# Optimization experiments

Hardware: AMD Instinct MI355X
Metric: run time of the kernel (lower is better)

Reference implementation:

```python
import jax, jax.numpy as jnp
import numpy as np

B, S, E, H = 2, 2048, 1024, 16
D = E // H  # head_dim = 64


def _rope(x):
    # x: (B, H, S, D); torchtune-style interleaved rotary embedding
    s, d = x.shape[-2], x.shape[-1]
    inv_freq = 1.0 / (10000.0 ** (jnp.arange(0, d, 2, dtype=jnp.float32) / d))  # (d/2,)
    freqs = jnp.arange(s, dtype=jnp.float32)[:, None] * inv_freq[None, :]       # (S, d/2)
    cos, sin = jnp.cos(freqs), jnp.sin(freqs)
    x1, x2 = x[..., 0::2], x[..., 1::2]
    o1 = x1 * cos - x2 * sin
    o2 = x2 * cos + x1 * sin
    return jnp.stack([o1, o2], axis=-1).reshape(x.shape)


def setup_inputs() -> dict:
    key = jax.random.key(0)
    kx, kq, kk, kv, ko = jax.random.split(key, 5)
    std = 1.0 / np.sqrt(E)
    return {
        "x": jax.random.normal(kx, (B, S, E), dtype=jnp.float32),
        "W_q": jax.random.normal(kq, (E, E), dtype=jnp.float32) * std,
        "W_k": jax.random.normal(kk, (E, E), dtype=jnp.float32) * std,
        "W_v": jax.random.normal(kv, (E, E), dtype=jnp.float32) * std,
        "W_o": jax.random.normal(ko, (E, E), dtype=jnp.float32) * std,
    }


def reference(x, W_q, W_k, W_v, W_o):
    b, s, e = x.shape
    h, d = H, e // H
    # nn.Linear: y = x @ W.T  (weights are (out, in))
    q = (x @ W_q.T).reshape(b, s, h, d).transpose(0, 2, 1, 3)  # (B,H,S,D)
    k = (x @ W_k.T).reshape(b, s, h, d).transpose(0, 2, 1, 3)
    v = (x @ W_v.T).reshape(b, s, h, d).transpose(0, 2, 1, 3)
    q = _rope(q)
    k = _rope(k)
    attn_scale = 1.0 / np.sqrt(e)  # NOTE: scales by sqrt(hidden_dim), as in source
    scores = jnp.einsum("bhsd,bhtd->bhst", q, k) * attn_scale  # (B,H,S,S)
    causal = jnp.triu(jnp.ones((s, s), dtype=bool), k=1)
    scores = jnp.where(causal, -jnp.inf, scores)
    probs = jax.nn.softmax(scores, axis=-1)  # dropout is identity in eval
    out = jnp.einsum("bhst,bhtd->bhsd", probs, v)
    out = out.transpose(0, 2, 1, 3).reshape(b, s, e)
    return out @ W_o.T
```

## Files before the change

### kernel.cpp

```cpp
#include <hip/hip_runtime.h>
#include <hip/hip_bf16.h>

#define BATCH 2
#define SEQ   2048
#define EMB   1024
#define NH    16
#define HD    64
#define MROWS (BATCH*SEQ)
#define NX    (MROWS*EMB)
#define NW    (EMB*EMB)

using f32x4  = __attribute__((ext_vector_type(4))) float;
using bf16x8 = __attribute__((ext_vector_type(8))) short;

#define GLOBAL_AS(p) ((const __attribute__((address_space(1))) void*)(p))
#define LDS_AS(p)    ((__attribute__((address_space(3))) void*)(p))

#define ROPE_L2 0.4152410118609203f
#define QSCALE  0.045084220027780106f

__global__ void fused_cast_kernel(const float* __restrict__ x,
                                  const float* __restrict__ Wq,
                                  const float* __restrict__ Wk,
                                  const float* __restrict__ Wv,
                                  const float* __restrict__ Wo,
                                  __hip_bfloat16* __restrict__ xb,
                                  __hip_bfloat16* __restrict__ Wqkvb,
                                  __hip_bfloat16* __restrict__ Wob,
                                  float2* __restrict__ ctab) {
    if (blockIdx.x >= 4096) {
        int e  = (blockIdx.x - 4096) * 256 + threadIdx.x;
        int s  = e >> 5;
        int ip = e & 31;
        float inv = exp2f(-(float)ip * ROPE_L2);
        float fr  = (float)s * inv;
        float2 cs;
        cs.x = cosf(fr);
        cs.y = sinf(fr);
        ctab[e] = cs;
        return;
    }
    size_t i8 = (size_t)(blockIdx.x * 256 + threadIdx.x) * 8;
    const float* src;
    __hip_bfloat16* dst;
    if (i8 < (size_t)NX) {
        src = x + i8;
        dst = xb + i8;
    } else {
        size_t w = i8 - NX;
        int which = (int)(w >> 20);
        size_t local = w & (NW - 1);
        if (which < 3) {
            src = (which == 0 ? Wq : (which == 1 ? Wk : Wv)) + local;
            dst = Wqkvb + w;
        } else {
            src = Wo + local;
            dst = Wob + local;
        }
    }
    float4 a = *(const float4*)(src);
    float4 b = *(const float4*)(src + 4);
    union { uint4 u; ushort s[8]; } o;
    const float* f = (const float*)&a;
#pragma unroll
    for (int j = 0; j < 4; ++j) {
        __hip_bfloat16 h = __float2bfloat16(f[j]);
        o.s[j] = *(ushort*)&h;
    }
    f = (const float*)&b;
#pragma unroll
    for (int j = 0; j < 4; ++j) {
        __hip_bfloat16 h = __float2bfloat16(f[j]);
        o.s[4 + j] = *(ushort*)&h;
    }
    *(uint4*)dst = o.u;
}

__global__ __launch_bounds__(256) void gemm_qkv_kernel(
        const __hip_bfloat16* __restrict__ A,
        const __hip_bfloat16* __restrict__ W,
        __hip_bfloat16* __restrict__ Qo,
        __hip_bfloat16* __restrict__ Ko,
        __hip_bfloat16* __restrict__ Vo,
        const float2* __restrict__ ctab, int M, int K) {
    __shared__ __hip_bfloat16 As[128 * 64];
    __shared__ __hip_bfloat16 Bs[128 * 64];

    const int tid  = threadIdx.x;
    const int wave = tid >> 6;
    const int lane = tid & 63;
    const int quad = lane >> 4;
    const int l16  = lane & 15;
    const int m0   = blockIdx.y * 128;
    const int n0   = blockIdx.x * 128;
    const int wm   = (wave >> 1) * 64;
    const int wn   = (wave & 1) * 64;
    const int xr   = l16 & 7;

    f32x4 acc[4][4] = {};

    for (int k0 = 0; k0 < K; k0 += 64) {
#pragma unroll
        for (int it = 0; it < 4; ++it) {
            int flat = (wave * 4 + it) * 64 + lane;
            int row  = flat >> 3;
            int g    = (flat & 7) ^ (row & 7);
            const __hip_bfloat16* ga = A + (size_t)(m0 + row) * K + k0 + g * 8;
            const __hip_bfloat16* gb = W + (size_t)(n0 + row) * K + k0 + g * 8;
            __builtin_amdgcn_global_load_lds(GLOBAL_AS(ga),
                LDS_AS(As + (size_t)(wave * 4 + it) * 512), 16, 0, 0);
            __builtin_amdgcn_global_load_lds(GLOBAL_AS(gb),
                LDS_AS(Bs + (size_t)(wave * 4 + it) * 512), 16, 0, 0);
        }
        __syncthreads();

#pragma unroll
        for (int kk = 0; kk < 2; ++kk) {
            const int kg = (kk * 4 + quad) ^ xr;
            bf16x8 af[4], bfr[4];
#pragma unroll
            for (int i = 0; i < 4; ++i) {
                af[i]  = *(const bf16x8*)(&As[(wm + i * 16 + l16) * 64 + kg * 8]);
                bfr[i] = *(const bf16x8*)(&Bs[(wn + i * 16 + l16) * 64 + kg * 8]);
            }
#pragma unroll
            for (int i = 0; i < 4; ++i)
#pragma unroll
                for (int j = 0; j < 4; ++j)
                    acc[i][j] = __builtin_amdgcn_mfma_f32_16x16x32_bf16(
                        af[i], bfr[j], acc[i][j], 0, 0, 0);
        }
        __syncthreads();
    }

    const int tens = n0 >> 10;
    __hip_bfloat16* outp = (tens == 0) ? Qo : ((tens == 1) ? Ko : Vo);
    const int nbase = n0 & 1023;
    if (tens < 2) {
        const float sgn   = (l16 & 1) ? 1.0f : -1.0f;
        const float qmul  = (tens == 0) ? QSCALE : 1.0f;
#pragma unroll
        for (int i = 0; i < 4; ++i)
#pragma unroll
            for (int j = 0; j < 4; ++j) {
                int col  = nbase + wn + j * 16 + l16;
                int ip   = ((wn + j * 16 + l16) & 63) >> 1;
                int row0 = m0 + wm + i * 16 + quad * 4;
#pragma unroll
                for (int rr = 0; rr < 4; ++rr) {
                    float v = acc[i][j][rr];
                    float p = __shfl_xor(v, 1);
                    int sp  = (row0 + rr) & (SEQ - 1);
                    float2 cs = ctab[sp * 32 + ip];
                    float o = (v * cs.x + sgn * p * cs.y) * qmul;
                    outp[(size_t)(row0 + rr) * EMB + col] = __float2bfloat16(o);
                }
            }
    } else {
#pragma unroll
        for (int i = 0; i < 4; ++i)
#pragma unroll
            for (int j = 0; j < 4; ++j) {
                int col  = nbase + wn + j * 16 + l16;
                int row0 = m0 + wm + i * 16 + quad * 4;
#pragma unroll
                for (int rr = 0; rr < 4; ++rr)
                    outp[(size_t)(row0 + rr) * EMB + col] = __float2bfloat16(acc[i][j][rr]);
            }
    }
}

__global__ __launch_bounds__(256) void gemm_oproj_kernel(
        const __hip_bfloat16* __restrict__ A,
        const __hip_bfloat16* __restrict__ Bm,
        float* __restrict__ C, int M, int N, int K) {
    __shared__ __hip_bfloat16 As[128 * 64];
    __shared__ __hip_bfloat16 Bs[64 * 64];

    const int tid  = threadIdx.x;
    const int wave = tid >> 6;
    const int lane = tid & 63;
    const int quad = lane >> 4;
    const int l16  = lane & 15;
    const int m0   = blockIdx.y * 128;
    const int n0   = blockIdx.x * 64;
    const int wm   = (wave >> 1) * 64;
    const int wn   = (wave & 1) * 32;
    const int xr   = l16 & 7;

    f32x4 acc[4][2] = {};

    for (int k0 = 0; k0 < K; k0 += 64) {
#pragma unroll
        for (int it = 0; it < 4; ++it) {
            int flat = (wave * 4 + it) * 64 + lane;
            int row  = flat >> 3;
            int g    = (flat & 7) ^ (row & 7);
            const __hip_bfloat16* ga = A + (size_t)(m0 + row) * K + k0 + g * 8;
            __builtin_amdgcn_global_load_lds(GLOBAL_AS(ga),
                LDS_AS(As + (size_t)(wave * 4 + it) * 512), 16, 0, 0);
        }
#pragma unroll
        for (int it = 0; it < 2; ++it) {
            int flat = (wave * 2 + it) * 64 + lane;
            int row  = flat >> 3;
            int g    = (flat & 7) ^ (row & 7);
            const __hip_bfloat16* gb = Bm + (size_t)(n0 + row) * K + k0 + g * 8;
            __builtin_amdgcn_global_load_lds(GLOBAL_AS(gb),
                LDS_AS(Bs + (size_t)(wave * 2 + it) * 512), 16, 0, 0);
        }
        __syncthreads();

#pragma unroll
        for (int kk = 0; kk < 2; ++kk) {
            const int kg = (kk * 4 + quad) ^ xr;
            bf16x8 af[4], bfr[2];
#pragma unroll
            for (int i = 0; i < 4; ++i)
                af[i] = *(const bf16x8*)(&As[(wm + i * 16 + l16) * 64 + kg * 8]);
#pragma unroll
            for (int j = 0; j < 2; ++j)
                bfr[j] = *(const bf16x8*)(&Bs[(wn + j * 16 + l16) * 64 + kg * 8]);
#pragma unroll
            for (int i = 0; i < 4; ++i)
#pragma unroll
                for (int j = 0; j < 2; ++j)
                    acc[i][j] = __builtin_amdgcn_mfma_f32_16x16x32_bf16(
                        af[i], bfr[j], acc[i][j], 0, 0, 0);
        }
        __syncthreads();
    }

#pragma unroll
    for (int i = 0; i < 4; ++i)
#pragma unroll
        for (int j = 0; j < 2; ++j) {
            int col  = n0 + wn + j * 16 + l16;
            int row0 = m0 + wm + i * 16 + quad * 4;
#pragma unroll
            for (int rr = 0; rr < 4; ++rr)
                C[(size_t)(row0 + rr) * N + col] = acc[i][j][rr];
        }
}

__device__ inline uint cvt_pk_bf16(float lo, float hi) {
    uint r;
    asm("v_cvt_pk_bf16_f32 %0, %1, %2" : "=v"(r) : "v"(lo), "v"(hi));
    return r;
}
__device__ inline float exp2_raw(float x) {
    float r;
    asm("v_exp_f32 %0, %1" : "=v"(r) : "v"(x));
    return r;
}

__global__ __launch_bounds__(512) void attn_mfma_kernel(
        const __hip_bfloat16* __restrict__ Qb,
        const __hip_bfloat16* __restrict__ Kb,
        const __hip_bfloat16* __restrict__ Vb,
        __hip_bfloat16* __restrict__ Attnb) {
    const int di   = blockIdx.y * 16 + blockIdx.x;
    const int qt   = 15 - (di >> 5);
    const int bh   = di & 31;
    const int b    = bh >> 4;
    const int h    = bh & (NH - 1);
    const int tid  = threadIdx.x;
    const int wave = tid >> 6;
    const int lane = tid & 63;
    const int quad = lane >> 4;
    const int l16  = lane & 15;

    __shared__ __hip_bfloat16 Ks[2][64 * 64];
    __shared__ uint VTs[2][64][33];

    const int pc   = tid >> 4;
    const int sgg  = tid & 15;
    const int d0   = sgg * 4;
    const int lr   = lane >> 3;
    const int lg   = (lane & 7) ^ lr;
    const size_t ksrc_lane = (size_t)lr * EMB + lg * 8;

    const __hip_bfloat16* Kbase = Kb + (size_t)b * SEQ * EMB + h * HD;
    const __hip_bfloat16* Vbase = Vb + (size_t)b * SEQ * EMB + h * HD;

    union { uint u[4]; bf16x8 v; } onesu;
    onesu.u[0] = 0x3F803F80u; onesu.u[1] = 0x3F803F80u;
    onesu.u[2] = 0x3F803F80u; onesu.u[3] = 0x3F803F80u;
    const bf16x8 ones = onesu.v;

    const int  nt      = 2 * qt + 2;
    const bool lowHalf = (wave < 4);
    const int  we      = lowHalf ? wave : wave - 4;

    const int qrow0 = qt * 128 + wave * 16;
    bf16x8 qf[2];
    {
        const __hip_bfloat16* qp =
            Qb + (size_t)(b * SEQ + qrow0 + l16) * EMB + h * HD + quad * 8;
        qf[0] = *(const bf16x8*)(qp);
        qf[1] = *(const bf16x8*)(qp + 32);
    }

    f32x4 of[4]  = {};
    f32x4 of_sum = {};

    const __hip_bfloat16* kgp = Kbase;
    const __hip_bfloat16* vgp = Vbase + (size_t)(2 * pc) * EMB + d0;
    uint2 va = *(const uint2*)(vgp);
    uint2 vb = *(const uint2*)(vgp + EMB);
    __builtin_amdgcn_global_load_lds(
        GLOBAL_AS(kgp + (size_t)(8 * wave) * EMB + ksrc_lane),
        LDS_AS(&Ks[0][wave * 512]), 16, 0, 0);

    for (int i = 0; i < nt; ++i) {
        const int cur = i & 1;

        {
            const uint* vau = (const uint*)&va;
            const uint* vbu = (const uint*)&vb;
#pragma unroll
            for (int j = 0; j < 2; ++j) {
                VTs[cur][d0 + 2 * j][pc] =
                    __builtin_amdgcn_perm(vbu[j], vau[j], 0x05040100u);
                VTs[cur][d0 + 2 * j + 1][pc] =
                    __builtin_amdgcn_perm(vbu[j], vau[j], 0x07060302u);
            }
        }
        __syncthreads();

        if (i + 1 < nt) {
            kgp += (size_t)64 * EMB;
            vgp += (size_t)64 * EMB;
            va = *(const uint2*)(vgp);
            vb = *(const uint2*)(vgp + EMB);
            __builtin_amdgcn_global_load_lds(
                GLOBAL_AS(kgp + (size_t)(8 * wave) * EMB + ksrc_lane),
                LDS_AS(&Ks[cur ^ 1][wave * 512]), 16, 0, 0);
        }

        const bool diagA = (i == 2 * qt);
        const bool diagB = (i == 2 * qt + 1);
        const bool skip  = diagB && lowHalf;
        if (skip) continue;
        const bool masking = (diagA && lowHalf) || (diagB && !lowHalf);

        const __hip_bfloat16* KsC = Ks[cur];
        f32x4 sc[4];
        __builtin_amdgcn_s_setprio(1);
#pragma unroll
        for (int mb = 0; mb < 4; ++mb) {
            f32x4 a = {};
            if (!(masking && mb > we)) {
                int krow = mb * 16 + l16;
#pragma unroll
                for (int kb = 0; kb < 2; ++kb) {
                    int kg = (kb * 4 + quad) ^ (krow & 7);
                    bf16x8 kf = *(const bf16x8*)(&KsC[krow * 64 + kg * 8]);
                    a = __builtin_amdgcn_mfma_f32_16x16x32_bf16(kf, qf[kb], a, 0, 0, 0);
                }
            }
            sc[mb] = a;
        }
        __builtin_amdgcn_s_setprio(0);

        if (masking) {
#pragma unroll
            for (int mb = 0; mb < 4; ++mb)
#pragma unroll
                for (int r = 0; r < 4; ++r)
                    if (mb * 16 + quad * 4 + r > we * 16 + l16)
                        sc[mb][r] = -16384.0f;
        }

#pragma unroll
        for (int mb = 0; mb < 4; ++mb)
#pragma unroll
            for (int r = 0; r < 4; ++r)
                sc[mb][r] = exp2_raw(sc[mb][r]);

        bf16x8 pf[2];
        {
            union { uint u[4]; bf16x8 v; } t;
            t.u[0] = cvt_pk_bf16(sc[0][0], sc[0][1]);
            t.u[1] = cvt_pk_bf16(sc[0][2], sc[0][3]);
            t.u[2] = cvt_pk_bf16(sc[1][0], sc[1][1]);
            t.u[3] = cvt_pk_bf16(sc[1][2], sc[1][3]);
            pf[0] = t.v;
            t.u[0] = cvt_pk_bf16(sc[2][0], sc[2][1]);
            t.u[1] = cvt_pk_bf16(sc[2][2], sc[2][3]);
            t.u[2] = cvt_pk_bf16(sc[3][0], sc[3][1]);
            t.u[3] = cvt_pk_bf16(sc[3][2], sc[3][3]);
            pf[1] = t.v;
        }

        const uint* VT0 = &VTs[cur][0][0];
        __builtin_amdgcn_s_setprio(1);
#pragma unroll
        for (int nb = 0; nb < 4; ++nb) {
            const uint* vrow = VT0 + (size_t)(nb * 16 + l16) * 33;
#pragma unroll
            for (int c = 0; c < 2; ++c) {
                union { uint u[4]; bf16x8 v; } vf;
                vf.u[0] = vrow[c * 16 + 2 * quad];
                vf.u[1] = vrow[c * 16 + 2 * quad + 1];
                vf.u[2] = vrow[c * 16 + 8 + 2 * quad];
                vf.u[3] = vrow[c * 16 + 8 + 2 * quad + 1];
                of[nb] = __builtin_amdgcn_mfma_f32_16x16x32_bf16(
                    pf[c], vf.v, of[nb], 0, 0, 0);
            }
        }
        of_sum = __builtin_amdgcn_mfma_f32_16x16x32_bf16(pf[0], ones, of_sum, 0, 0, 0);
        of_sum = __builtin_amdgcn_mfma_f32_16x16x32_bf16(pf[1], ones, of_sum, 0, 0, 0);
        __builtin_amdgcn_s_setprio(0);
    }

    const int rl0 = quad * 4;
    float linv[4];
#pragma unroll
    for (int r = 0; r < 4; ++r)
        linv[r] = 1.0f / of_sum[r];
#pragma unroll
    for (int nb = 0; nb < 4; ++nb)
#pragma unroll
        for (int r = 0; r < 4; ++r) {
            float v = of[nb][r] * linv[r];
            Attnb[(size_t)(b * SEQ + qrow0 + rl0 + r) * EMB + h * HD + nb * 16 + l16] =
                __float2bfloat16(v);
        }
}

extern "C" void kernel_launch(void* const* d_in, const int* in_sizes, int n_in,
                              void* d_out, int out_size, void* d_ws, size_t ws_size,
                              hipStream_t stream) {
    const float* x  = (const float*)d_in[0];
    const float* Wq = (const float*)d_in[1];
    const float* Wk = (const float*)d_in[2];
    const float* Wv = (const float*)d_in[3];
    const float* Wo = (const float*)d_in[4];
    float* out = (float*)d_out;

    char* ws = (char*)d_ws;
    size_t off = 0;
    auto alloc = [&](size_t bytes) -> void* {
        void* p = ws + off;
        off += (bytes + 255) & ~(size_t)255;
        return p;
    };

    __hip_bfloat16* xb    = (__hip_bfloat16*)alloc((size_t)NX * 2);
    __hip_bfloat16* Wqkvb = (__hip_bfloat16*)alloc((size_t)NW * 3 * 2);
    __hip_bfloat16* Wob   = (__hip_bfloat16*)alloc((size_t)NW * 2);
    __hip_bfloat16* Qbuf  = (__hip_bfloat16*)alloc((size_t)NX * 2);
    __hip_bfloat16* Kbuf  = (__hip_bfloat16*)alloc((size_t)NX * 2);
    __hip_bfloat16* Vbuf  = (__hip_bfloat16*)alloc((size_t)NX * 2);
    __hip_bfloat16* Attnb = (__hip_bfloat16*)alloc((size_t)NX * 2);
    float2*         ctab  = (float2*)alloc((size_t)SEQ * 32 * sizeof(float2));

    fused_cast_kernel<<<(NX + 4 * NW) / (256 * 8) + 256, 256, 0, stream>>>(
        x, Wq, Wk, Wv, Wo, xb, Wqkvb, Wob, ctab);

    dim3 qgrid(24, MROWS / 128);
    gemm_qkv_kernel<<<qgrid, 256, 0, stream>>>(xb, Wqkvb, Qbuf, Kbuf, Vbuf,
                                               ctab, MROWS, EMB);

    dim3 agrid(16, 32);
    attn_mfma_kernel<<<agrid, 512, 0, stream>>>(Qbuf, Kbuf, Vbuf, Attnb);

    dim3 ggrid(EMB / 64, MROWS / 128);
    gemm_oproj_kernel<<<ggrid, 256, 0, stream>>>(Attnb, Wob, out, MROWS, EMB, EMB);
}
```

Before: 193.1 us.

## Double-buffer QKV GEMM with 256x256 tiles and 512-thread blocks

The QKV projection GEMM moves from 128x128 tiles with 256 threads and one LDS buffer to 256x256 tiles with 512 threads and 128KB of dynamic LDS split into two buffers. The global-to-LDS loads for the next K step are issued before computing the current one, which drops one barrier per iteration and overlaps load latency with MFMA work. Each wave now computes a 128x64 sub-tile, which raises data reuse per LDS fragment. The trade-offs are only 192 blocks for 256 CUs, large LDS use that limits residency to one block per CU, and higher register pressure from the doubled accumulator array.

Result: faster. 185.6 us (-3.9%).

```diff
diff --git a/kernel.cpp b/kernel.cpp
--- a/kernel.cpp
+++ b/kernel.cpp
@@ -76,59 +76,82 @@
     *(uint4*)dst = o.u;
 }
 
-__global__ __launch_bounds__(256) void gemm_qkv_kernel(
+__global__ __launch_bounds__(512, 2) void gemm_qkv_kernel(
         const __hip_bfloat16* __restrict__ A,
         const __hip_bfloat16* __restrict__ W,
         __hip_bfloat16* __restrict__ Qo,
         __hip_bfloat16* __restrict__ Ko,
         __hip_bfloat16* __restrict__ Vo,
         const float2* __restrict__ ctab, int M, int K) {
-    __shared__ __hip_bfloat16 As[128 * 64];
-    __shared__ __hip_bfloat16 Bs[128 * 64];
+    extern __shared__ __hip_bfloat16 smem[];
 
     const int tid  = threadIdx.x;
     const int wave = tid >> 6;
     const int lane = tid & 63;
     const int quad = lane >> 4;
     const int l16  = lane & 15;
-    const int m0   = blockIdx.y * 128;
-    const int n0   = blockIdx.x * 128;
-    const int wm   = (wave >> 1) * 64;
-    const int wn   = (wave & 1) * 64;
-    const int xr   = l16 & 7;
-
-    f32x4 acc[4][4] = {};
-
-    for (int k0 = 0; k0 < K; k0 += 64) {
-#pragma unroll
-        for (int it = 0; it < 4; ++it) {
-            int flat = (wave * 4 + it) * 64 + lane;
-            int row  = flat >> 3;
-            int g    = (flat & 7) ^ (row & 7);
-            const __hip_bfloat16* ga = A + (size_t)(m0 + row) * K + k0 + g * 8;
-            const __hip_bfloat16* gb = W + (size_t)(n0 + row) * K + k0 + g * 8;
-            __builtin_amdgcn_global_load_lds(GLOBAL_AS(ga),
-                LDS_AS(As + (size_t)(wave * 4 + it) * 512), 16, 0, 0);
-            __builtin_amdgcn_global_load_lds(GLOBAL_AS(gb),
-                LDS_AS(Bs + (size_t)(wave * 4 + it) * 512), 16, 0, 0);
-        }
-        __syncthreads();
-
-#pragma unroll
-        for (int kk = 0; kk < 2; ++kk) {
-            const int kg = (kk * 4 + quad) ^ xr;
-            bf16x8 af[4], bfr[4];
-#pragma unroll
-            for (int i = 0; i < 4; ++i) {
-                af[i]  = *(const bf16x8*)(&As[(wm + i * 16 + l16) * 64 + kg * 8]);
-                bfr[i] = *(const bf16x8*)(&Bs[(wn + i * 16 + l16) * 64 + kg * 8]);
-            }
-#pragma unroll
-            for (int i = 0; i < 4; ++i)
-#pragma unroll
-                for (int j = 0; j < 4; ++j)
-                    acc[i][j] = __builtin_amdgcn_mfma_f32_16x16x32_bf16(
-                        af[i], bfr[j], acc[i][j], 0, 0, 0);
+    const int m0   = blockIdx.y * 256;
+    const int n0   = blockIdx.x * 256;
+    const int mw   = wave >> 2;
+    const int nw   = wave & 3;
+
+    const int lr   = lane >> 3;
+    const int lg   = (lane & 7) ^ lr;
+    const bool stA = (wave < 4);
+    const int srow = (stA ? wave : wave - 4) * 64;
+    const __hip_bfloat16* gbase =
+        (stA ? A + (size_t)(m0 + srow) * K : W + (size_t)(n0 + srow) * K)
+        + (size_t)lr * K + lg * 8;
+    const int dbase = (stA ? 0 : 32768) + srow * 64;
+
+    f32x4 acc[8][4] = {};
+
+    const int nkt = K >> 6;
+
+#pragma unroll
+    for (int t = 0; t < 8; ++t)
+        __builtin_amdgcn_global_load_lds(
+            GLOBAL_AS(gbase + (size_t)(t * 8) * K),
+            LDS_AS(smem + dbase + t * 512), 16, 0, 0);
+    __syncthreads();
+
+    for (int it = 0; it < nkt; ++it) {
+        const int cur = it & 1;
+        if (it + 1 < nkt) {
+            const __hip_bfloat16* gs = gbase + (size_t)(it + 1) * 64;
+            __hip_bfloat16* dn = smem + dbase + (cur ? 0 : 16384);
+#pragma unroll
+            for (int t = 0; t < 8; ++t)
+                __builtin_amdgcn_global_load_lds(
+                    GLOBAL_AS(gs + (size_t)(t * 8) * K),
+                    LDS_AS(dn + t * 512), 16, 0, 0);
+        }
+
+        const __hip_bfloat16* Ac = smem + (cur ? 16384 : 0);
+        const __hip_bfloat16* Bc = smem + 32768 + (cur ? 16384 : 0);
+#pragma unroll
+        for (int ks = 0; ks < 2; ++ks) {
+            bf16x8 bq[4];
+#pragma unroll
+            for (int j = 0; j < 4; ++j) {
+                int br = nw * 64 + j * 16 + l16;
+                bq[j] = *(const bf16x8*)(Bc + br * 64 + (((ks * 4 + quad) ^ (br & 7)) * 8));
+            }
+#pragma unroll
+            for (int ih = 0; ih < 2; ++ih) {
+                bf16x8 aq[4];
+#pragma unroll
+                for (int i2 = 0; i2 < 4; ++i2) {
+                    int ar = mw * 128 + (ih * 4 + i2) * 16 + l16;
+                    aq[i2] = *(const bf16x8*)(Ac + ar * 64 + (((ks * 4 + quad) ^ (ar & 7)) * 8));
+                }
+#pragma unroll
+                for (int i2 = 0; i2 < 4; ++i2)
+#pragma unroll
+                    for (int j = 0; j < 4; ++j)
+                        acc[ih * 4 + i2][j] = __builtin_amdgcn_mfma_f32_16x16x32_bf16(
+                            aq[i2], bq[j], acc[ih * 4 + i2][j], 0, 0, 0);
+            }
         }
         __syncthreads();
     }
@@ -137,15 +160,15 @@
     __hip_bfloat16* outp = (tens == 0) ? Qo : ((tens == 1) ? Ko : Vo);
     const int nbase = n0 & 1023;
     if (tens < 2) {
-        const float sgn   = (l16 & 1) ? 1.0f : -1.0f;
-        const float qmul  = (tens == 0) ? QSCALE : 1.0f;
-#pragma unroll
-        for (int i = 0; i < 4; ++i)
+        const float sgn  = (l16 & 1) ? 1.0f : -1.0f;
+        const float qmul = (tens == 0) ? QSCALE : 1.0f;
+#pragma unroll
+        for (int i = 0; i < 8; ++i)
 #pragma unroll
             for (int j = 0; j < 4; ++j) {
-                int col  = nbase + wn + j * 16 + l16;
-                int ip   = ((wn + j * 16 + l16) & 63) >> 1;
-                int row0 = m0 + wm + i * 16 + quad * 4;
+                int col  = nbase + nw * 64 + j * 16 + l16;
+                int ip   = (col & 63) >> 1;
+                int row0 = m0 + mw * 128 + i * 16 + quad * 4;
 #pragma unroll
                 for (int rr = 0; rr < 4; ++rr) {
                     float v = acc[i][j][rr];
@@ -158,11 +181,11 @@
             }
     } else {
 #pragma unroll
-        for (int i = 0; i < 4; ++i)
+        for (int i = 0; i < 8; ++i)
 #pragma unroll
             for (int j = 0; j < 4; ++j) {
-                int col  = nbase + wn + j * 16 + l16;
-                int row0 = m0 + wm + i * 16 + quad * 4;
+                int col  = nbase + nw * 64 + j * 16 + l16;
+                int row0 = m0 + mw * 128 + i * 16 + quad * 4;
 #pragma unroll
                 for (int rr = 0; rr < 4; ++rr)
                     outp[(size_t)(row0 + rr) * EMB + col] = __float2bfloat16(acc[i][j][rr]);
@@ -456,12 +479,20 @@
     __hip_bfloat16* Attnb = (__hip_bfloat16*)alloc((size_t)NX * 2);
     float2*         ctab  = (float2*)alloc((size_t)SEQ * 32 * sizeof(float2));
 
+    static bool attrDone = false;
+    if (!attrDone) {
+        (void)hipFuncSetAttribute((const void*)gemm_qkv_kernel,
+                                  hipFuncAttributeMaxDynamicSharedMemorySize,
+                                  131072);
+        attrDone = true;
+    }
+
     fused_cast_kernel<<<(NX + 4 * NW) / (256 * 8) + 256, 256, 0, stream>>>(
         x, Wq, Wk, Wv, Wo, xb, Wqkvb, Wob, ctab);
 
-    dim3 qgrid(24, MROWS / 128);
-    gemm_qkv_kernel<<<qgrid, 256, 0, stream>>>(xb, Wqkvb, Qbuf, Kbuf, Vbuf,
-                                               ctab, MROWS, EMB);
+    dim3 qgrid(3072 / 256, MROWS / 256);
+    gemm_qkv_kernel<<<qgrid, 512, 131072, stream>>>(xb, Wqkvb, Qbuf, Kbuf, Vbuf,
+                                                    ctab, MROWS, EMB);
 
     dim3 agrid(16, 32);
     attn_mfma_kernel<<<agrid, 512, 0, stream>>>(Qbuf, Kbuf, Vbuf, Attnb);
```
